# Kernel optimization log

Measured on AMD Instinct MI355X. Metric: run time of the kernel, lower is better.

Reference implementation:

```python
import jax, jax.numpy as jnp
import numpy as np

N = 16384          # batch of utterance embeddings
D = 512            # embedding dim
NUM_CLASSES = 256  # speakers; labels are contiguous 0..C-1 (required by S[i, y[i]] indexing)
EPS_NORM = 1e-12   # F.normalize eps
EPS_COS = 1e-8     # F.cosine_similarity eps


def setup_inputs() -> dict:
    key = jax.random.key(0)
    emb = jax.random.normal(key, (N, D), dtype=jnp.float32)
    # arange % C guarantees every class has exactly N//C (=64) samples (>=2 needed for exclusion centroid)
    y = (jnp.arange(N, dtype=jnp.int32) % NUM_CLASSES).astype(jnp.int32)
    w = jnp.float32(10.0)
    b = jnp.float32(-5.0)
    return {"emb": emb, "y": y, "w": w, "b": b}


def _cosine_sim_matrix(e, y):
    # e: [N, D] already L2-normalized. Per-class centroid sums via segment reduce.
    csum = jax.ops.segment_sum(e, y, num_segments=NUM_CLASSES)                     # [C, D]
    counts = jax.ops.segment_sum(jnp.ones((N,), e.dtype), y, num_segments=NUM_CLASSES)  # [C]
    e_norm = jnp.linalg.norm(e, axis=1)                                            # [N] (~1)

    # Other-class similarity: cos(e_i, centroid_k / n_k) for all k
    cen = csum / counts[:, None]                                                   # [C, D]
    cen_norm = jnp.linalg.norm(cen, axis=1)                                        # [C]
    sim_other = (e @ cen.T) / jnp.maximum(e_norm[:, None] * cen_norm[None, :], EPS_COS)  # [N, C]

    # Same-class similarity: exclude e_i from its own centroid
    cen_self = (csum[y] - e) / (counts[y] - 1.0)[:, None]                          # [N, D]
    self_norm = jnp.linalg.norm(cen_self, axis=1)                                  # [N]
    sim_self = jnp.sum(e * cen_self, axis=1) / jnp.maximum(e_norm * self_norm, EPS_COS)  # [N]

    is_own = y[:, None] == jnp.arange(NUM_CLASSES, dtype=y.dtype)[None, :]         # [N, C]
    return jnp.where(is_own, sim_self[:, None], sim_other)


def reference(emb, y, w, b):
    # e = F.normalize(emb, p=2, dim=1)
    e = emb / jnp.maximum(jnp.linalg.norm(emb, axis=1, keepdims=True), EPS_NORM)
    sim = _cosine_sim_matrix(e, y) * w + b                                         # [N, C]
    # softmax embed loss: -log_softmax over dim=0 (batch axis, as in the original code)
    nls = -jax.nn.log_softmax(sim, axis=0)                                         # [N, C]
    L = nls[jnp.arange(N), y]                                                      # [N]
    return L.sum()
```

## Files before the change

### kernel.cpp

```cpp
#include <hip/hip_runtime.h>
#include <math.h>
#include <stdint.h>


typedef __attribute__((ext_vector_type(8))) short bf16x8;
typedef __attribute__((ext_vector_type(4))) float f32x4;
struct alignas(16) US8 { unsigned short u[8]; };

__device__ inline float waveReduceSum(float v) {
#pragma unroll
    for (int m = 32; m >= 1; m >>= 1) v += __shfl_xor(v, m, 64);
    return v;
}
__device__ inline unsigned short f2bf(float f) {
    uint32_t u = __float_as_uint(f);
    return (unsigned short)((u + 0x7FFFu + ((u >> 16) & 1u)) >> 16);
}
__device__ inline void gload_lds16(const void* g, void* l) {
    __builtin_amdgcn_global_load_lds(
        (const __attribute__((address_space(1))) uint32_t*)g,
        (__attribute__((address_space(3))) uint32_t*)l, 16, 0, 0);
}

__global__ __launch_bounds__(1024) void k_centroid(
        const float* __restrict__ emb, const int* __restrict__ y,
        const float* __restrict__ wptr, unsigned short* __restrict__ ebf,
        unsigned short* __restrict__ csum_bf, float* __restrict__ normsq,
        float* __restrict__ colscale, int* __restrict__ counts, int N) {
    __shared__ float part[16][512];
    __shared__ float red[512];
    __shared__ int cnts[16];
    int c = blockIdx.x;
    int tid = threadIdx.x, l = tid & 63, w = tid >> 6;
    int chunk = N >> 4;
    float facc[8] = {0.f, 0.f, 0.f, 0.f, 0.f, 0.f, 0.f, 0.f};
    int cnt = 0;
    int iend = (w + 1) * chunk;
    int i0 = w * chunk;
    int4 y4 = *reinterpret_cast<const int4*>(y + i0 + l * 4);
    for (; i0 < iend; i0 += 256) {
        int4 cy = y4;
        if (i0 + 256 < iend)
            y4 = *reinterpret_cast<const int4*>(y + i0 + 256 + l * 4);
#pragma unroll
        for (int comp = 0; comp < 4; ++comp) {
            int yv = (comp == 0) ? cy.x : (comp == 1) ? cy.y : (comp == 2) ? cy.z : cy.w;
            unsigned long long m = __ballot(yv == c);
            cnt += (int)__popcll(m);
            while (m) {
                int b = __builtin_ctzll(m);
                m &= m - 1;
                int r = i0 + 4 * b + comp;
                const float4* pr = reinterpret_cast<const float4*>(emb + (size_t)r * 512);
                float4 v0 = pr[l * 2], v1 = pr[l * 2 + 1];
                float s = v0.x * v0.x + v0.y * v0.y + v0.z * v0.z + v0.w * v0.w
                        + v1.x * v1.x + v1.y * v1.y + v1.z * v1.z + v1.w * v1.w;
                s = waveReduceSum(s);
                float inv = 1.0f / fmaxf(sqrtf(s), 1e-12f);
                float e0 = v0.x * inv, e1 = v0.y * inv, e2 = v0.z * inv, e3 = v0.w * inv;
                float e4 = v1.x * inv, e5 = v1.y * inv, e6 = v1.z * inv, e7 = v1.w * inv;
                US8 t;
                t.u[0] = f2bf(e0); t.u[1] = f2bf(e1); t.u[2] = f2bf(e2); t.u[3] = f2bf(e3);
                t.u[4] = f2bf(e4); t.u[5] = f2bf(e5); t.u[6] = f2bf(e6); t.u[7] = f2bf(e7);
                *reinterpret_cast<US8*>(ebf + (size_t)r * 512 + l * 8) = t;
                facc[0] += e0; facc[1] += e1; facc[2] += e2; facc[3] += e3;
                facc[4] += e4; facc[5] += e5; facc[6] += e6; facc[7] += e7;
            }
        }
    }
    *reinterpret_cast<float4*>(&part[w][l * 8]) =
        make_float4(facc[0], facc[1], facc[2], facc[3]);
    *reinterpret_cast<float4*>(&part[w][l * 8 + 4]) =
        make_float4(facc[4], facc[5], facc[6], facc[7]);
    if (l == 0) cnts[w] = cnt;
    __syncthreads();
    if (tid < 512) {
        float s = 0.f;
#pragma unroll
        for (int r = 0; r < 16; ++r) s += part[r][tid];
        csum_bf[(size_t)c * 512 + tid] = f2bf(s);
        red[tid] = s * s;
    }
    __syncthreads();
    for (int o = 256; o >= 1; o >>= 1) {
        if (tid < o) red[tid] += red[tid + o];
        __syncthreads();
    }
    if (tid == 0) {
        int ct = 0;
#pragma unroll
        for (int r = 0; r < 16; ++r) ct += cnts[r];
        counts[c] = ct;
        float nsq = red[0];
        normsq[c] = nsq;
        colscale[c] = wptr[0] / fmaxf(sqrtf(nsq), (float)ct * 1e-8f);
    }
}

#define NKT 8

__global__ __launch_bounds__(512) void k_gemm(
        const unsigned short* __restrict__ ebf, const unsigned short* __restrict__ csum_bf,
        const int* __restrict__ y, const float* __restrict__ colscale,
        const float* __restrict__ normsq, const int* __restrict__ counts,
        const float* __restrict__ wptr, const float* __restrict__ bptr,
        float* __restrict__ colpart, float* __restrict__ selfpart, int C) {
    __shared__ __align__(16) unsigned short As[2][8 * 512];
    __shared__ __align__(16) unsigned short Bs[2][32 * 512];
    __shared__ float colsum[256];
    __shared__ float selfred[8];

    const int tid = threadIdx.x;
    const int l = tid & 63;
    const int w = tid >> 6;
    const int bx = blockIdx.x;
    const int r0 = bx * 64;
    const int rsub = l >> 2;
    const int kcs = ((l & 3) ^ ((l >> 3) & 3)) * 8;

    const unsigned short* srcA = ebf + (size_t)(r0 + (w & 3) * 16 + rsub) * 512
                               + (w >> 2) * 32 + kcs;
    const unsigned short* srcB[4];
#pragma unroll
    for (int i = 0; i < 4; ++i) {
        int st = w * 4 + i;
        srcB[i] = csum_bf + (size_t)((st & 15) * 16 + rsub) * 512 + (st >> 4) * 32 + kcs;
    }
    const int fro = (l & 15) * 32 + (((l >> 4) ^ ((l >> 1) & 3)) * 8);

    f32x4 acc[4][2];
#pragma unroll
    for (int m = 0; m < 4; ++m)
#pragma unroll
        for (int n = 0; n < 2; ++n) acc[m][n] = (f32x4){0.f, 0.f, 0.f, 0.f};

    gload_lds16(srcA, &As[0][w * 512]);
#pragma unroll
    for (int i = 0; i < 4; ++i) gload_lds16(srcB[i], &Bs[0][(w * 4 + i) * 512]);
    __syncthreads();

    int cur = 0;
    for (int kt = 0; kt < NKT; ++kt) {
        if (kt + 1 < NKT) {
            gload_lds16(srcA + (kt + 1) * 64, &As[cur ^ 1][w * 512]);
#pragma unroll
            for (int i = 0; i < 4; ++i)
                gload_lds16(srcB[i] + (kt + 1) * 64, &Bs[cur ^ 1][(w * 4 + i) * 512]);
        }
#pragma unroll
        for (int h = 0; h < 2; ++h) {
            bf16x8 af[4];
#pragma unroll
            for (int m = 0; m < 4; ++m)
                af[m] = *reinterpret_cast<const bf16x8*>(&As[cur][(h * 4 + m) * 512 + fro]);
#pragma unroll
            for (int n = 0; n < 2; ++n) {
                bf16x8 bv = *reinterpret_cast<const bf16x8*>(
                    &Bs[cur][(h * 16 + w * 2 + n) * 512 + fro]);
#pragma unroll
                for (int m = 0; m < 4; ++m)
                    acc[m][n] = __builtin_amdgcn_mfma_f32_16x16x32_bf16(af[m], bv, acc[m][n], 0, 0, 0);
            }
        }
        __syncthreads();
        cur ^= 1;
    }

    float bv = bptr[0], wv = wptr[0];
    int lcol = l & 15, lrow4 = (l >> 4) * 4;
    float cs[2], nsq[2], cm1[2]; int cls[2];
#pragma unroll
    for (int n = 0; n < 2; ++n) {
        int c = w * 32 + n * 16 + lcol;
        cls[n] = c; cs[n] = colscale[c]; nsq[n] = normsq[c];
        cm1[n] = (float)(counts[c] - 1);
    }
    float colacc[2] = {0.f, 0.f};
    float selfacc = 0.f;
#pragma unroll
    for (int m = 0; m < 4; ++m) {
#pragma unroll
        for (int j = 0; j < 4; ++j) {
            int row = r0 + m * 16 + lrow4 + j;
            int yc = y[row];
#pragma unroll
            for (int n = 0; n < 2; ++n) {
                float dot = acc[m][n][j];
                float logit;
                if (yc == cls[n]) {
                    float un2 = fmaxf(nsq[n] - 2.f * dot + 1.f, 0.f);
                    float denom = fmaxf(sqrtf(un2), cm1[n] * 1e-8f);
                    logit = wv * (dot - 1.f) / denom + bv;
                    selfacc += logit;
                } else {
                    logit = dot * cs[n] + bv;
                }
                colacc[n] += __expf(logit);
            }
        }
    }
#pragma unroll
    for (int n = 0; n < 2; ++n) {
        float v = colacc[n];
        v += __shfl_xor(v, 16, 64);
        v += __shfl_xor(v, 32, 64);
        colacc[n] = v;
    }
    selfacc = waveReduceSum(selfacc);
    if (l < 16) {
#pragma unroll
        for (int n = 0; n < 2; ++n) colsum[w * 32 + n * 16 + l] = colacc[n];
    }
    if (l == 0) selfred[w] = selfacc;
    __syncthreads();
    if (tid < 256)
        colpart[(size_t)bx * 256 + tid] = colsum[tid];
    if (tid == 0)
        selfpart[bx] = selfred[0] + selfred[1] + selfred[2] + selfred[3]
                     + selfred[4] + selfred[5] + selfred[6] + selfred[7];
}

__global__ __launch_bounds__(64) void k_colreduce(
        const float* __restrict__ colpart, const int* __restrict__ counts,
        float* __restrict__ contrib, int nbx, int C) {
    int c = blockIdx.x, l = threadIdx.x;
    float s = 0.f;
    for (int i = l; i < nbx; i += 64) s += colpart[(size_t)i * C + c];
    s = waveReduceSum(s);
    if (l == 0) contrib[c] = (float)counts[c] * logf(s);
}

__global__ __launch_bounds__(256) void k_final(
        const float* __restrict__ contrib, const float* __restrict__ selfpart,
        float* __restrict__ out, int nbx, int C) {
    __shared__ float lds[256];
    int tid = threadIdx.x;
    float v = (tid < C) ? contrib[tid] : 0.f;
    for (int i = tid; i < nbx; i += 256) v -= selfpart[i];
    lds[tid] = v;
    __syncthreads();
    for (int o = 128; o >= 1; o >>= 1) {
        if (tid < o) lds[tid] += lds[tid + o];
        __syncthreads();
    }
    if (tid == 0) out[0] = lds[0];
}

extern "C" void kernel_launch(void* const* d_in, const int* in_sizes, int n_in,
                              void* d_out, int out_size, void* d_ws, size_t ws_size,
                              hipStream_t stream) {
    const float* emb  = (const float*)d_in[0];
    const int*   y    = (const int*)d_in[1];
    const float* wptr = (const float*)d_in[2];
    const float* bptr = (const float*)d_in[3];
    float* out = (float*)d_out;
    int N = in_sizes[1];
    const int C = 256;
    int nbx = N / 64;

    unsigned short* ebf     = (unsigned short*)d_ws;
    unsigned short* csum_bf = ebf + (size_t)N * 512;
    float* colpart  = (float*)(csum_bf + (size_t)C * 512);
    float* selfpart = colpart + (size_t)nbx * C;
    float* normsq   = selfpart + nbx;
    float* colscale = normsq + C;
    int*   counts   = (int*)(colscale + C);
    float* contrib  = (float*)(counts + C);

    k_centroid <<<C, 1024, 0, stream>>>(emb, y, wptr, ebf, csum_bf, normsq,
                                        colscale, counts, N);
    k_gemm     <<<nbx, 512, 0, stream>>>(ebf, csum_bf, y, colscale, normsq, counts,
                                         wptr, bptr, colpart, selfpart, C);
    k_colreduce<<<C, 64, 0, stream>>>(colpart, counts, contrib, nbx, C);
    k_final    <<<1, 256, 0, stream>>>(contrib, selfpart, out, nbx, C);
}
```

Before: 35.64 us.

## Drop bf16 embedding materialization; normalize and convert fp32 rows inside GEMM

The centroid kernel no longer writes a normalized bf16 copy of the embeddings (16 MB of stores). It stores only per-row inverse norms. The GEMM kernel now reads fp32 embeddings directly through registers, scales and converts them to bf16, and writes them to LDS after the MFMA work of each step. This cuts a global write and read pass, but the GEMM now reads twice as many bytes for A and uses register-staged loads instead of direct-to-LDS loads, which adds VALU conversion work and register pressure.

```diff
diff --git a/kernel.cpp b/kernel.cpp
--- a/kernel.cpp
+++ b/kernel.cpp
@@ -24,7 +24,7 @@
 
 __global__ __launch_bounds__(1024) void k_centroid(
         const float* __restrict__ emb, const int* __restrict__ y,
-        const float* __restrict__ wptr, unsigned short* __restrict__ ebf,
+        const float* __restrict__ wptr, float* __restrict__ inv_norm,
         unsigned short* __restrict__ csum_bf, float* __restrict__ normsq,
         float* __restrict__ colscale, int* __restrict__ counts, int N) {
     __shared__ float part[16][512];
@@ -57,14 +57,11 @@
                         + v1.x * v1.x + v1.y * v1.y + v1.z * v1.z + v1.w * v1.w;
                 s = waveReduceSum(s);
                 float inv = 1.0f / fmaxf(sqrtf(s), 1e-12f);
-                float e0 = v0.x * inv, e1 = v0.y * inv, e2 = v0.z * inv, e3 = v0.w * inv;
-                float e4 = v1.x * inv, e5 = v1.y * inv, e6 = v1.z * inv, e7 = v1.w * inv;
-                US8 t;
-                t.u[0] = f2bf(e0); t.u[1] = f2bf(e1); t.u[2] = f2bf(e2); t.u[3] = f2bf(e3);
-                t.u[4] = f2bf(e4); t.u[5] = f2bf(e5); t.u[6] = f2bf(e6); t.u[7] = f2bf(e7);
-                *reinterpret_cast<US8*>(ebf + (size_t)r * 512 + l * 8) = t;
-                facc[0] += e0; facc[1] += e1; facc[2] += e2; facc[3] += e3;
-                facc[4] += e4; facc[5] += e5; facc[6] += e6; facc[7] += e7;
+                if (l == 0) inv_norm[r] = inv;
+                facc[0] += v0.x * inv; facc[1] += v0.y * inv;
+                facc[2] += v0.z * inv; facc[3] += v0.w * inv;
+                facc[4] += v1.x * inv; facc[5] += v1.y * inv;
+                facc[6] += v1.z * inv; facc[7] += v1.w * inv;
             }
         }
     }
@@ -100,7 +97,8 @@
 #define NKT 8
 
 __global__ __launch_bounds__(512) void k_gemm(
-        const unsigned short* __restrict__ ebf, const unsigned short* __restrict__ csum_bf,
+        const float* __restrict__ emb, const float* __restrict__ inv_norm,
+        const unsigned short* __restrict__ csum_bf,
         const int* __restrict__ y, const float* __restrict__ colscale,
         const float* __restrict__ normsq, const int* __restrict__ counts,
         const float* __restrict__ wptr, const float* __restrict__ bptr,
@@ -118,8 +116,9 @@
     const int rsub = l >> 2;
     const int kcs = ((l & 3) ^ ((l >> 3) & 3)) * 8;
 
-    const unsigned short* srcA = ebf + (size_t)(r0 + (w & 3) * 16 + rsub) * 512
-                               + (w >> 2) * 32 + kcs;
+    const int arow = r0 + (w & 3) * 16 + rsub;
+    const float* srcA = emb + (size_t)arow * 512 + (w >> 2) * 32 + kcs;
+    const float invA = inv_norm[arow];
     const unsigned short* srcB[4];
 #pragma unroll
     for (int i = 0; i < 4; ++i) {
@@ -134,15 +133,27 @@
 #pragma unroll
         for (int n = 0; n < 2; ++n) acc[m][n] = (f32x4){0.f, 0.f, 0.f, 0.f};
 
-    gload_lds16(srcA, &As[0][w * 512]);
+    {
+        float4 a0 = *reinterpret_cast<const float4*>(srcA);
+        float4 a1 = *reinterpret_cast<const float4*>(srcA + 4);
+        US8 t;
+        t.u[0] = f2bf(a0.x * invA); t.u[1] = f2bf(a0.y * invA);
+        t.u[2] = f2bf(a0.z * invA); t.u[3] = f2bf(a0.w * invA);
+        t.u[4] = f2bf(a1.x * invA); t.u[5] = f2bf(a1.y * invA);
+        t.u[6] = f2bf(a1.z * invA); t.u[7] = f2bf(a1.w * invA);
+        *reinterpret_cast<US8*>(&As[0][w * 512 + l * 8]) = t;
+    }
 #pragma unroll
     for (int i = 0; i < 4; ++i) gload_lds16(srcB[i], &Bs[0][(w * 4 + i) * 512]);
     __syncthreads();
 
     int cur = 0;
     for (int kt = 0; kt < NKT; ++kt) {
-        if (kt + 1 < NKT) {
-            gload_lds16(srcA + (kt + 1) * 64, &As[cur ^ 1][w * 512]);
+        float4 a0, a1;
+        const bool hasNext = (kt + 1 < NKT);
+        if (hasNext) {
+            a0 = *reinterpret_cast<const float4*>(srcA + (kt + 1) * 64);
+            a1 = *reinterpret_cast<const float4*>(srcA + (kt + 1) * 64 + 4);
 #pragma unroll
             for (int i = 0; i < 4; ++i)
                 gload_lds16(srcB[i] + (kt + 1) * 64, &Bs[cur ^ 1][(w * 4 + i) * 512]);
@@ -161,6 +172,14 @@
                 for (int m = 0; m < 4; ++m)
                     acc[m][n] = __builtin_amdgcn_mfma_f32_16x16x32_bf16(af[m], bv, acc[m][n], 0, 0, 0);
             }
+        }
+        if (hasNext) {
+            US8 t;
+            t.u[0] = f2bf(a0.x * invA); t.u[1] = f2bf(a0.y * invA);
+            t.u[2] = f2bf(a0.z * invA); t.u[3] = f2bf(a0.w * invA);
+            t.u[4] = f2bf(a1.x * invA); t.u[5] = f2bf(a1.y * invA);
+            t.u[6] = f2bf(a1.z * invA); t.u[7] = f2bf(a1.w * invA);
+            *reinterpret_cast<US8*>(&As[cur ^ 1][w * 512 + l * 8]) = t;
         }
         __syncthreads();
         cur ^= 1;
@@ -258,8 +277,8 @@
     const int C = 256;
     int nbx = N / 64;
 
-    unsigned short* ebf     = (unsigned short*)d_ws;
-    unsigned short* csum_bf = ebf + (size_t)N * 512;
+    float* inv_norm = (float*)d_ws;
+    unsigned short* csum_bf = (unsigned short*)(inv_norm + N);
     float* colpart  = (float*)(csum_bf + (size_t)C * 512);
     float* selfpart = colpart + (size_t)nbx * C;
     float* normsq   = selfpart + nbx;
@@ -267,10 +286,10 @@
     int*   counts   = (int*)(colscale + C);
     float* contrib  = (float*)(counts + C);
 
-    k_centroid <<<C, 1024, 0, stream>>>(emb, y, wptr, ebf, csum_bf, normsq,
+    k_centroid <<<C, 1024, 0, stream>>>(emb, y, wptr, inv_norm, csum_bf, normsq,
                                         colscale, counts, N);
-    k_gemm     <<<nbx, 512, 0, stream>>>(ebf, csum_bf, y, colscale, normsq, counts,
-                                         wptr, bptr, colpart, selfpart, C);
+    k_gemm     <<<nbx, 512, 0, stream>>>(emb, inv_norm, csum_bf, y, colscale, normsq,
+                                         counts, wptr, bptr, colpart, selfpart, C);
     k_colreduce<<<C, 64, 0, stream>>>(colpart, counts, contrib, nbx, C);
     k_final    <<<1, 256, 0, stream>>>(contrib, selfpart, out, nbx, C);
 }
```

Measured after the change: 33.63 us. 5.6% less time.
